# Optimization experiments

Hardware: AMD Instinct MI355X
Metric: run time of the kernel (lower is better)

Reference implementation:

```python
import jax, jax.numpy as jnp
import numpy as np

B, H, S, D = 4, 16, 2048, 128


def setup_inputs() -> dict:
    key = jax.random.key(0)
    kq, kk, kv = jax.random.split(key, 3)
    query = jax.random.normal(kq, (B, H, S, D), dtype=jnp.float32)
    key_t = jax.random.normal(kk, (B, H, S, D), dtype=jnp.float32)
    value = jax.random.normal(kv, (B, H, S, D), dtype=jnp.float32)
    # causal mask, broadcast over batch and heads: True = keep
    mask = jnp.tril(jnp.ones((S, S), dtype=bool))[None, None].repeat(B, 0).repeat(H, 1)
    return {"query": query, "key": key_t, "value": value, "mask": mask}


def reference(query, key, value, mask):
    scale = 1.0 / np.sqrt(D).astype(np.float32)
    # [b,h,sq,sk] scores
    scores = jnp.einsum("bhqd,bhkd->bhqk", query, key) * scale
    scores = jnp.where(mask, scores, -jnp.inf)
    probs = jax.nn.softmax(scores, axis=-1)
    return jnp.einsum("bhqk,bhkd->bhqd", probs, value)
```

## Files before the change

kernel.cpp:

```cpp
#include <hip/hip_runtime.h>


#define SLEN 2048
#define DDIM 128
#define NBH  64
#define QB   256
#define KB   64

typedef __bf16 bf16x8 __attribute__((ext_vector_type(8)));
typedef float  f32x16 __attribute__((ext_vector_type(16)));
typedef float  f32x4  __attribute__((ext_vector_type(4)));
typedef unsigned uint32x4 __attribute__((ext_vector_type(4)));
typedef unsigned short ushort_t;
typedef ushort_t ushort8 __attribute__((ext_vector_type(8)));

__device__ inline ushort_t f2bf(float f) {
  union { float f; unsigned u; } v; v.f = f;
  unsigned u = v.u;
  u += 0x7FFFu + ((u >> 16) & 1u);
  return (ushort_t)(u >> 16);
}

__device__ inline unsigned cvtpk_bf16(float lo, float hi) {
  unsigned r;
  asm("v_cvt_pk_bf16_f32 %0, %1, %2" : "=v"(r) : "v"(lo), "v"(hi));
  return r;
}

__device__ inline float exp2_fast(float x) {
  float r;
  asm("v_exp_f32 %0, %1" : "=v"(r) : "v"(x));
  return r;
}

__global__ __launch_bounds__(256) void convert_k_kernel(
    const float* __restrict__ in, ushort_t* __restrict__ out, int n4) {
  int stride = gridDim.x * blockDim.x;
  for (int i = blockIdx.x * blockDim.x + threadIdx.x; i < n4; i += stride) {
    float4 x = reinterpret_cast<const float4*>(in)[i];
    unsigned lo = (unsigned)f2bf(x.x) | ((unsigned)f2bf(x.y) << 16);
    unsigned hi = (unsigned)f2bf(x.z) | ((unsigned)f2bf(x.w) << 16);
    reinterpret_cast<uint2*>(out)[i] = make_uint2(lo, hi);
  }
}

__global__ __launch_bounds__(256) void transpose_v_kernel(
    const float* __restrict__ V, ushort_t* __restrict__ Vt) {
  __shared__ float t[64][33];
  const int bh = blockIdx.z;
  const int s0 = blockIdx.x * 64;
  const int d0 = blockIdx.y * 32;
  const int tx = threadIdx.x & 31;
  const int ty = threadIdx.x >> 5;
  const float* src = V + ((size_t)bh * SLEN + s0) * DDIM + d0;
#pragma unroll
  for (int j = 0; j < 8; ++j) {
    int sl = ty + j * 8;
    t[sl][tx] = src[(size_t)sl * DDIM + tx];
  }
  __syncthreads();
  ushort_t* dst = Vt + ((size_t)bh * DDIM + d0) * SLEN + s0;
#pragma unroll
  for (int j = 0; j < 4; ++j) {
    int dl = ty + j * 8;
    unsigned lo = f2bf(t[tx * 2][dl]);
    unsigned hi = f2bf(t[tx * 2 + 1][dl]);
    *reinterpret_cast<unsigned*>(&dst[(size_t)dl * SLEN + tx * 2]) =
        lo | (hi << 16);
  }
}

__global__ __launch_bounds__(512, 2) void fattn4_kernel(
    const float* __restrict__ Q, const ushort_t* __restrict__ Kb,
    const ushort_t* __restrict__ Vt, float* __restrict__ Out) {
  __shared__ ushort_t K_sh[2][KB * DDIM];
  __shared__ ushort_t V_sh[2][DDIM * KB];

  const int tid  = threadIdx.x;
  const int lane = tid & 63;
  const int wv   = tid >> 6;
  const int l31  = lane & 31;
  const int hi   = lane >> 5;
  const int qblk = (blockIdx.y >= 32) ? blockIdx.x : (7 - (int)blockIdx.x);
  const int bh   = blockIdx.y;

  const float qscale = 0.12751744f;
  const float THR = 11.0f;

  const float*    Qp = Q  + (size_t)bh * SLEN * DDIM;
  const ushort_t* Kp = Kb + (size_t)bh * SLEN * DDIM;
  const ushort_t* Vp = Vt + (size_t)bh * DDIM * SLEN;
  float*          Op = Out + (size_t)bh * SLEN * DDIM;

  const int q0w = qblk * QB + wv * 32;
  const int qg  = q0w + l31;

  bf16x8 qf[8];
  {
    const float* qr = Qp + (size_t)qg * DDIM;
#pragma unroll
    for (int ds = 0; ds < 8; ++ds) {
      int d0 = ds * 16 + hi * 8;
      float4 x = *reinterpret_cast<const float4*>(qr + d0);
      float4 y = *reinterpret_cast<const float4*>(qr + d0 + 4);
      ushort8 uu;
      uu[0] = f2bf(x.x * qscale); uu[1] = f2bf(x.y * qscale);
      uu[2] = f2bf(x.z * qscale); uu[3] = f2bf(x.w * qscale);
      uu[4] = f2bf(y.x * qscale); uu[5] = f2bf(y.y * qscale);
      uu[6] = f2bf(y.z * qscale); uu[7] = f2bf(y.w * qscale);
      qf[ds] = __builtin_bit_cast(bf16x8, uu);
    }
  }

  f32x16 Oacc[4];
#pragma unroll
  for (int dt = 0; dt < 4; ++dt)
#pragma unroll
    for (int r = 0; r < 16; ++r) Oacc[dt][r] = 0.f;
  float m_run = -3.0e38f, l_run = 0.f;

  const int last_kb      = qblk * 4 + 3;
  const int last_kb_wave = (q0w + 31) >> 6;

  auto stage = [&](int buf, int kb) {
    const ushort_t* ksrc = Kp + (size_t)kb * KB * DDIM;
#pragma unroll
    for (int j = 0; j < 2; ++j) {
      int chunk = wv * 128 + j * 64 + lane;
      int row = chunk >> 4, c = chunk & 15;
      const ushort_t* g = ksrc + row * DDIM + ((c ^ (row & 7)) << 3);
      ushort_t* l = &K_sh[buf][(size_t)(wv * 128 + j * 64) * 8];
      __builtin_amdgcn_global_load_lds(
          (const __attribute__((address_space(1))) unsigned*)g,
          (__attribute__((address_space(3))) unsigned*)l, 16, 0, 0);
    }
    const ushort_t* vsrc = Vp + (size_t)kb * KB;
#pragma unroll
    for (int j = 0; j < 2; ++j) {
      int chunk = wv * 128 + j * 64 + lane;
      int row = chunk >> 3, c = chunk & 7;
      const ushort_t* g = vsrc + (size_t)row * SLEN + ((c ^ (row & 7)) << 3);
      ushort_t* l = &V_sh[buf][(size_t)(wv * 128 + j * 64) * 8];
      __builtin_amdgcn_global_load_lds(
          (const __attribute__((address_space(1))) unsigned*)g,
          (__attribute__((address_space(3))) unsigned*)l, 16, 0, 0);
    }
  };

  stage(0, 0);

  for (int kb = 0; kb <= last_kb; ++kb) {
    __syncthreads();
    if (kb < last_kb) stage((kb + 1) & 1, kb + 1);

    if (kb <= last_kb_wave) {
      const int buf = kb & 1;

      f32x16 sac[2];
#pragma unroll
      for (int mt = 0; mt < 2; ++mt) {
        f32x16 a;
#pragma unroll
        for (int r = 0; r < 16; ++r) a[r] = 0.f;
        int row = mt * 32 + l31;
        int sw = row & 7;
        __builtin_amdgcn_s_setprio(1);
#pragma unroll
        for (int ds = 0; ds < 8; ++ds) {
          int c = ds * 2 + hi;
          bf16x8 kf = *reinterpret_cast<const bf16x8*>(
              &K_sh[buf][row * DDIM + ((c ^ sw) << 3)]);
          a = __builtin_amdgcn_mfma_f32_32x32x16_bf16(kf, qf[ds], a, 0, 0, 0);
        }
        __builtin_amdgcn_s_setprio(0);
        sac[mt] = a;
      }

      if (kb * 64 + 63 > q0w) {
#pragma unroll
        for (int mt = 0; mt < 2; ++mt) {
          int kbase = kb * 64 + mt * 32 + 4 * hi;
#pragma unroll
          for (int r = 0; r < 16; ++r) {
            int krow = (r & 3) + 8 * (r >> 2);
            if (kbase + krow > qg) sac[mt][r] = -3.0e38f;
          }
        }
      }

      float p0 = sac[0][0], p1 = sac[0][1], p2 = sac[0][2], p3 = sac[0][3];
#pragma unroll
      for (int r = 4; r < 16; r += 4) {
        p0 = fmaxf(p0, sac[0][r + 0]); p1 = fmaxf(p1, sac[0][r + 1]);
        p2 = fmaxf(p2, sac[0][r + 2]); p3 = fmaxf(p3, sac[0][r + 3]);
      }
#pragma unroll
      for (int r = 0; r < 16; r += 4) {
        p0 = fmaxf(p0, sac[1][r + 0]); p1 = fmaxf(p1, sac[1][r + 1]);
        p2 = fmaxf(p2, sac[1][r + 2]); p3 = fmaxf(p3, sac[1][r + 3]);
      }
      float tm = fmaxf(fmaxf(p0, p1), fmaxf(p2, p3));
      tm = fmaxf(tm, __shfl_xor(tm, 32));

      if (!__all(tm - m_run <= THR)) {
        float mnew  = fmaxf(m_run, tm);
        float alpha = exp2_fast(m_run - mnew);
        m_run = mnew;
        l_run *= alpha;
#pragma unroll
        for (int dt = 0; dt < 4; ++dt)
#pragma unroll
          for (int r = 0; r < 16; ++r) Oacc[dt][r] *= alpha;
      }

      float s0 = 0.f, s1 = 0.f, s2 = 0.f, s3 = 0.f;
#pragma unroll
      for (int mt = 0; mt < 2; ++mt)
#pragma unroll
        for (int r = 0; r < 16; r += 4) {
          float e0 = exp2_fast(sac[mt][r + 0] - m_run);
          float e1 = exp2_fast(sac[mt][r + 1] - m_run);
          float e2 = exp2_fast(sac[mt][r + 2] - m_run);
          float e3 = exp2_fast(sac[mt][r + 3] - m_run);
          sac[mt][r + 0] = e0; sac[mt][r + 1] = e1;
          sac[mt][r + 2] = e2; sac[mt][r + 3] = e3;
          s0 += e0; s1 += e1; s2 += e2; s3 += e3;
        }
      float rs = (s0 + s1) + (s2 + s3);
      rs += __shfl_xor(rs, 32);
      l_run += rs;

      uint32x4 pw[4];
#pragma unroll
      for (int ks = 0; ks < 4; ++ks) {
        const int mt = ks >> 1;
        const int hb = 8 * (ks & 1);
        unsigned X  = cvtpk_bf16(sac[mt][hb + 0], sac[mt][hb + 1]);
        unsigned X2 = cvtpk_bf16(sac[mt][hb + 2], sac[mt][hb + 3]);
        unsigned Y  = cvtpk_bf16(sac[mt][hb + 4], sac[mt][hb + 5]);
        unsigned Y2 = cvtpk_bf16(sac[mt][hb + 6], sac[mt][hb + 7]);
        asm("v_permlane32_swap_b32 %0, %1" : "+v"(X),  "+v"(Y));
        asm("v_permlane32_swap_b32 %0, %1" : "+v"(X2), "+v"(Y2));
        uint32x4 f; f.x = X; f.y = X2; f.z = Y; f.w = Y2;
        pw[ks] = f;
      }

#pragma unroll
      for (int dt = 0; dt < 4; ++dt) {
        int row = dt * 32 + l31;
        int sw = row & 7;
        __builtin_amdgcn_s_setprio(1);
#pragma unroll
        for (int ks = 0; ks < 4; ++ks) {
          int c = ks * 2 + hi;
          bf16x8 vf = *reinterpret_cast<const bf16x8*>(
              &V_sh[buf][row * 64 + ((c ^ sw) << 3)]);
          Oacc[dt] = __builtin_amdgcn_mfma_f32_32x32x16_bf16(
              vf, __builtin_bit_cast(bf16x8, pw[ks]), Oacc[dt], 0, 0, 0);
        }
        __builtin_amdgcn_s_setprio(0);
      }
    }
  }

  {
    float invl = 1.0f / l_run;
    float* orow = Op + (size_t)qg * DDIM;
#pragma unroll
    for (int dt = 0; dt < 4; ++dt)
#pragma unroll
      for (int r = 0; r < 16; ++r) {
        int d = dt * 32 + (r & 3) + 8 * (r >> 2) + 4 * hi;
        orow[d] = Oacc[dt][r] * invl;
      }
  }
}

__global__ __launch_bounds__(256) void fattn_kernel(
    const float* __restrict__ Q, const float* __restrict__ K,
    const float* __restrict__ V, float* __restrict__ Out) {
  __shared__ ushort_t K_sh[64 * 128];
  __shared__ ushort_t V_sh[128 * 64];
  __shared__ ushort_t P_sh[4][16 * 64];

  const int tid  = threadIdx.x;
  const int lane = tid & 63;
  const int wv   = tid >> 6;
  const int l16  = lane & 15;
  const int lhi  = lane >> 4;
  const int qblk = blockIdx.x;
  const int bh   = blockIdx.y;
  const float scale = 0.08838834764831845f;

  const size_t base = (size_t)bh * SLEN * DDIM;
  const float* Qp = Q + base;
  const float* Kp = K + base;
  const float* Vp = V + base;
  float*       Op = Out + base;

  bf16x8 qf[4];
  {
    const int qrow = qblk * 64 + wv * 16 + l16;
    const float* qr = Qp + (size_t)qrow * DDIM;
#pragma unroll
    for (int dc = 0; dc < 4; ++dc) {
      int d0 = dc * 32 + lhi * 8;
      float4 x = *reinterpret_cast<const float4*>(qr + d0);
      float4 y = *reinterpret_cast<const float4*>(qr + d0 + 4);
      ushort8 uu;
      uu[0] = f2bf(x.x * scale); uu[1] = f2bf(x.y * scale);
      uu[2] = f2bf(x.z * scale); uu[3] = f2bf(x.w * scale);
      uu[4] = f2bf(y.x * scale); uu[5] = f2bf(y.y * scale);
      uu[6] = f2bf(y.z * scale); uu[7] = f2bf(y.w * scale);
      qf[dc] = __builtin_bit_cast(bf16x8, uu);
    }
  }

  f32x4 Oacc[8];
#pragma unroll
  for (int i = 0; i < 8; ++i) Oacc[i] = (f32x4){0.f, 0.f, 0.f, 0.f};
  float m_run[4], l_run[4];
#pragma unroll
  for (int r = 0; r < 4; ++r) { m_run[r] = -3.0e38f; l_run[r] = 0.f; }

  for (int kb = 0; kb <= qblk; ++kb) {
    __syncthreads();
    {
      const float* src = Kp + (size_t)kb * 64 * DDIM;
#pragma unroll
      for (int it = 0; it < 8; ++it) {
        int idx4 = it * 256 + tid;
        int r  = idx4 >> 5;
        int c4 = idx4 & 31;
        float4 x = *reinterpret_cast<const float4*>(src + r * DDIM + c4 * 4);
        unsigned lo = ((unsigned)f2bf(x.y) << 16) | f2bf(x.x);
        unsigned hh = ((unsigned)f2bf(x.w) << 16) | f2bf(x.z);
        int e = (r * 128 + c4 * 4) ^ ((r & 7) << 3);
        *reinterpret_cast<uint2*>(&K_sh[e]) = make_uint2(lo, hh);
      }
      const float* vs = Vp + (size_t)kb * 64 * DDIM;
#pragma unroll
      for (int it = 0; it < 8; ++it) {
        int idx4 = it * 256 + tid;
        int r  = idx4 >> 5;
        int c4 = idx4 & 31;
        float4 x = *reinterpret_cast<const float4*>(vs + r * DDIM + c4 * 4);
        int c0 = c4 * 4;
        float vals[4] = {x.x, x.y, x.z, x.w};
#pragma unroll
        for (int j = 0; j < 4; ++j) {
          int d = c0 + j;
          V_sh[(d * 64 + r) ^ ((d & 7) << 3)] = f2bf(vals[j]);
        }
      }
    }
    __syncthreads();

    f32x4 sacc[4];
#pragma unroll
    for (int g = 0; g < 4; ++g) {
      f32x4 acc = (f32x4){0.f, 0.f, 0.f, 0.f};
#pragma unroll
      for (int dc = 0; dc < 4; ++dc) {
        int row = g * 16 + l16;
        int e = (row * 128 + dc * 32 + lhi * 8) ^ ((row & 7) << 3);
        bf16x8 kf = *reinterpret_cast<const bf16x8*>(&K_sh[e]);
        acc = __builtin_amdgcn_mfma_f32_16x16x32_bf16(qf[dc], kf, acc, 0, 0, 0);
      }
      sacc[g] = acc;
    }

    if (kb == qblk) {
      int q0 = lhi * 4;
#pragma unroll
      for (int g = 0; g < 4; ++g) {
        int kcol = g * 16 + l16;
#pragma unroll
        for (int r = 0; r < 4; ++r) {
          if (kcol > wv * 16 + q0 + r) sacc[g][r] = -3.0e38f;
        }
      }
    }

    float tmax[4];
#pragma unroll
    for (int r = 0; r < 4; ++r)
      tmax[r] = fmaxf(fmaxf(sacc[0][r], sacc[1][r]),
                      fmaxf(sacc[2][r], sacc[3][r]));
#pragma unroll
    for (int x = 1; x < 16; x <<= 1) {
#pragma unroll
      for (int r = 0; r < 4; ++r)
        tmax[r] = fmaxf(tmax[r], __shfl_xor(tmax[r], x));
    }

    float alpha[4], mnew[4];
#pragma unroll
    for (int r = 0; r < 4; ++r) {
      mnew[r]  = fmaxf(m_run[r], tmax[r]);
      alpha[r] = __expf(m_run[r] - mnew[r]);
      m_run[r] = mnew[r];
    }

    float rsum[4] = {0.f, 0.f, 0.f, 0.f};
#pragma unroll
    for (int g = 0; g < 4; ++g) {
#pragma unroll
      for (int r = 0; r < 4; ++r) {
        float p = __expf(sacc[g][r] - mnew[r]);
        rsum[r] += p;
        int prow = lhi * 4 + r;
        P_sh[wv][(prow * 64 + g * 16 + l16) ^ ((prow & 7) << 3)] = f2bf(p);
      }
    }
#pragma unroll
    for (int x = 1; x < 16; x <<= 1) {
#pragma unroll
      for (int r = 0; r < 4; ++r) rsum[r] += __shfl_xor(rsum[r], x);
    }
#pragma unroll
    for (int r = 0; r < 4; ++r) l_run[r] = l_run[r] * alpha[r] + rsum[r];

#pragma unroll
    for (int dg = 0; dg < 8; ++dg)
#pragma unroll
      for (int r = 0; r < 4; ++r) Oacc[dg][r] *= alpha[r];

    bf16x8 pf[2];
#pragma unroll
    for (int kc = 0; kc < 2; ++kc) {
      int e = (l16 * 64 + kc * 32 + lhi * 8) ^ ((l16 & 7) << 3);
      pf[kc] = *reinterpret_cast<const bf16x8*>(&P_sh[wv][e]);
    }
#pragma unroll
    for (int dg = 0; dg < 8; ++dg) {
#pragma unroll
      for (int kc = 0; kc < 2; ++kc) {
        int row = dg * 16 + l16;
        int e = (row * 64 + kc * 32 + lhi * 8) ^ ((row & 7) << 3);
        bf16x8 vf = *reinterpret_cast<const bf16x8*>(&V_sh[e]);
        Oacc[dg] = __builtin_amdgcn_mfma_f32_16x16x32_bf16(pf[kc], vf, Oacc[dg], 0, 0, 0);
      }
    }
  }

#pragma unroll
  for (int r = 0; r < 4; ++r) {
    float inv = 1.0f / l_run[r];
    int q = qblk * 64 + wv * 16 + lhi * 4 + r;
    float* orow = Op + (size_t)q * DDIM;
#pragma unroll
    for (int dg = 0; dg < 8; ++dg)
      orow[dg * 16 + l16] = Oacc[dg][r] * inv;
  }
}

extern "C" void kernel_launch(void* const* d_in, const int* in_sizes, int n_in,
                              void* d_out, int out_size, void* d_ws, size_t ws_size,
                              hipStream_t stream) {
  const float* Q = (const float*)d_in[0];
  const float* K = (const float*)d_in[1];
  const float* V = (const float*)d_in[2];
  float* O = (float*)d_out;

  const size_t n_elem = (size_t)NBH * SLEN * DDIM;
  const size_t need   = n_elem * 2 * 2;

  if (ws_size >= need) {
    ushort_t* Kbf = (ushort_t*)d_ws;
    ushort_t* Vt  = Kbf + n_elem;
    convert_k_kernel<<<2048, 256, 0, stream>>>(K, Kbf, (int)(n_elem / 4));
    transpose_v_kernel<<<dim3(SLEN / 64, DDIM / 32, NBH), 256, 0, stream>>>(V, Vt);
    fattn4_kernel<<<dim3(SLEN / QB, NBH), dim3(512), 0, stream>>>(Q, Kbf, Vt, O);
  } else {
    fattn_kernel<<<dim3(SLEN / 64, NBH), dim3(256), 0, stream>>>(Q, K, V, O);
  }
}
```

Measured before the change: 143.1 us.

## Software-pipeline QK^T with softmax/PV across triple-buffered tiles and merge prepasses

Restructures the attention main loop so the QK^T MFMAs for tile t are issued before the softmax and PV work for tile t-1. K/V LDS staging goes from a double buffer to a triple buffer so prefetch, compute and finish can each use their own tile. The K convert and V transpose prepasses are merged into one launch, and the output store is vectorized to float4. The aim is to overlap matrix-core work with exp/reduction work and save a kernel launch, at the cost of more LDS and more live registers, which could cut occupancy.

```diff
diff --git a/kernel.cpp b/kernel.cpp
--- a/kernel.cpp
+++ b/kernel.cpp
@@ -33,48 +33,153 @@
   return r;
 }
 
-__global__ __launch_bounds__(256) void convert_k_kernel(
-    const float* __restrict__ in, ushort_t* __restrict__ out, int n4) {
-  int stride = gridDim.x * blockDim.x;
-  for (int i = blockIdx.x * blockDim.x + threadIdx.x; i < n4; i += stride) {
-    float4 x = reinterpret_cast<const float4*>(in)[i];
-    unsigned lo = (unsigned)f2bf(x.x) | ((unsigned)f2bf(x.y) << 16);
-    unsigned hi = (unsigned)f2bf(x.z) | ((unsigned)f2bf(x.w) << 16);
-    reinterpret_cast<uint2*>(out)[i] = make_uint2(lo, hi);
-  }
-}
-
-__global__ __launch_bounds__(256) void transpose_v_kernel(
-    const float* __restrict__ V, ushort_t* __restrict__ Vt) {
+__global__ __launch_bounds__(256) void prepass_kernel(
+    const float* __restrict__ K, const float* __restrict__ V,
+    ushort_t* __restrict__ Kb, ushort_t* __restrict__ Vt) {
   __shared__ float t[64][33];
-  const int bh = blockIdx.z;
-  const int s0 = blockIdx.x * 64;
-  const int d0 = blockIdx.y * 32;
-  const int tx = threadIdx.x & 31;
-  const int ty = threadIdx.x >> 5;
-  const float* src = V + ((size_t)bh * SLEN + s0) * DDIM + d0;
-#pragma unroll
-  for (int j = 0; j < 8; ++j) {
-    int sl = ty + j * 8;
-    t[sl][tx] = src[(size_t)sl * DDIM + tx];
-  }
-  __syncthreads();
-  ushort_t* dst = Vt + ((size_t)bh * DDIM + d0) * SLEN + s0;
-#pragma unroll
-  for (int j = 0; j < 4; ++j) {
-    int dl = ty + j * 8;
-    unsigned lo = f2bf(t[tx * 2][dl]);
-    unsigned hi = f2bf(t[tx * 2 + 1][dl]);
-    *reinterpret_cast<unsigned*>(&dst[(size_t)dl * SLEN + tx * 2]) =
-        lo | (hi << 16);
-  }
-}
-
-__global__ __launch_bounds__(512, 2) void fattn4_kernel(
+  if (blockIdx.x < 2048) {
+    const int n4 = (int)((size_t)NBH * SLEN * DDIM / 4);
+    const int stride = 2048 * 256;
+    for (int i = blockIdx.x * 256 + threadIdx.x; i < n4; i += stride) {
+      float4 x = reinterpret_cast<const float4*>(K)[i];
+      unsigned lo = (unsigned)f2bf(x.x) | ((unsigned)f2bf(x.y) << 16);
+      unsigned hi = (unsigned)f2bf(x.z) | ((unsigned)f2bf(x.w) << 16);
+      reinterpret_cast<uint2*>(Kb)[i] = make_uint2(lo, hi);
+    }
+  } else {
+    const int vb = (int)blockIdx.x - 2048;
+    const int bh = vb >> 7;
+    const int d0 = ((vb >> 5) & 3) * 32;
+    const int s0 = (vb & 31) * 64;
+    const int tx = threadIdx.x & 31;
+    const int ty = threadIdx.x >> 5;
+    const float* src = V + ((size_t)bh * SLEN + s0) * DDIM + d0;
+#pragma unroll
+    for (int j = 0; j < 8; ++j) {
+      int sl = ty + j * 8;
+      t[sl][tx] = src[(size_t)sl * DDIM + tx];
+    }
+    __syncthreads();
+    ushort_t* dst = Vt + ((size_t)bh * DDIM + d0) * SLEN + s0;
+#pragma unroll
+    for (int j = 0; j < 4; ++j) {
+      int dl = ty + j * 8;
+      unsigned lo = f2bf(t[tx * 2][dl]);
+      unsigned hi = f2bf(t[tx * 2 + 1][dl]);
+      *reinterpret_cast<unsigned*>(&dst[(size_t)dl * SLEN + tx * 2]) =
+          lo | (hi << 16);
+    }
+  }
+}
+
+#define QKT(S, TT) do {                                                      \
+    const int _b = (TT) % 3;                                                 \
+    _Pragma("unroll")                                                        \
+    for (int mt = 0; mt < 2; ++mt) {                                         \
+      f32x16 a;                                                              \
+      _Pragma("unroll")                                                      \
+      for (int r = 0; r < 16; ++r) a[r] = 0.f;                               \
+      int row = mt * 32 + l31;                                               \
+      int sw = row & 7;                                                      \
+      _Pragma("unroll")                                                      \
+      for (int ds = 0; ds < 8; ++ds) {                                       \
+        int c = ds * 2 + hi;                                                 \
+        bf16x8 kf = *reinterpret_cast<const bf16x8*>(                        \
+            &K_sh[_b][row * DDIM + ((c ^ sw) << 3)]);                        \
+        a = __builtin_amdgcn_mfma_f32_32x32x16_bf16(kf, qf[ds], a, 0, 0, 0); \
+      }                                                                      \
+      S[mt] = a;                                                             \
+    }                                                                        \
+  } while (0)
+
+#define FINISH(S, U) do {                                                    \
+    const int _u = (U);                                                      \
+    const int _vb = _u % 3;                                                  \
+    if (_u * 64 + 63 > q0w) {                                                \
+      _Pragma("unroll")                                                      \
+      for (int mt = 0; mt < 2; ++mt) {                                       \
+        int kbase = _u * 64 + mt * 32 + 4 * hi;                              \
+        _Pragma("unroll")                                                    \
+        for (int r = 0; r < 16; ++r) {                                       \
+          int krow = (r & 3) + 8 * (r >> 2);                                 \
+          if (kbase + krow > qg) S[mt][r] = -3.0e38f;                        \
+        }                                                                    \
+      }                                                                      \
+    }                                                                        \
+    float p0 = S[0][0], p1 = S[0][1], p2 = S[0][2], p3 = S[0][3];            \
+    _Pragma("unroll")                                                        \
+    for (int r = 4; r < 16; r += 4) {                                        \
+      p0 = fmaxf(p0, S[0][r]);     p1 = fmaxf(p1, S[0][r + 1]);              \
+      p2 = fmaxf(p2, S[0][r + 2]); p3 = fmaxf(p3, S[0][r + 3]);              \
+    }                                                                        \
+    _Pragma("unroll")                                                        \
+    for (int r = 0; r < 16; r += 4) {                                        \
+      p0 = fmaxf(p0, S[1][r]);     p1 = fmaxf(p1, S[1][r + 1]);              \
+      p2 = fmaxf(p2, S[1][r + 2]); p3 = fmaxf(p3, S[1][r + 3]);              \
+    }                                                                        \
+    float tm = fmaxf(fmaxf(p0, p1), fmaxf(p2, p3));                          \
+    tm = fmaxf(tm, __shfl_xor(tm, 32));                                      \
+    if (!__all(tm - m_run <= THR)) {                                         \
+      float mnew  = fmaxf(m_run, tm);                                        \
+      float alpha = exp2_fast(m_run - mnew);                                 \
+      m_run = mnew; l_run *= alpha;                                          \
+      _Pragma("unroll")                                                      \
+      for (int dt = 0; dt < 4; ++dt)                                         \
+        _Pragma("unroll")                                                    \
+        for (int r = 0; r < 16; ++r) Oacc[dt][r] *= alpha;                   \
+    }                                                                        \
+    float s0 = 0.f, s1 = 0.f, s2 = 0.f, s3 = 0.f;                            \
+    _Pragma("unroll")                                                        \
+    for (int mt = 0; mt < 2; ++mt)                                           \
+      _Pragma("unroll")                                                      \
+      for (int r = 0; r < 16; r += 4) {                                      \
+        float e0 = exp2_fast(S[mt][r + 0] - m_run);                          \
+        float e1 = exp2_fast(S[mt][r + 1] - m_run);                          \
+        float e2 = exp2_fast(S[mt][r + 2] - m_run);                          \
+        float e3 = exp2_fast(S[mt][r + 3] - m_run);                          \
+        S[mt][r + 0] = e0; S[mt][r + 1] = e1;                                \
+        S[mt][r + 2] = e2; S[mt][r + 3] = e3;                                \
+        s0 += e0; s1 += e1; s2 += e2; s3 += e3;                              \
+      }                                                                      \
+    float rs = (s0 + s1) + (s2 + s3);                                        \
+    rs += __shfl_xor(rs, 32);                                                \
+    l_run += rs;                                                             \
+    uint32x4 pw[4];                                                          \
+    _Pragma("unroll")                                                        \
+    for (int ks = 0; ks < 4; ++ks) {                                         \
+      const int mt = ks >> 1;                                                \
+      const int hb = 8 * (ks & 1);                                           \
+      unsigned X  = cvtpk_bf16(S[mt][hb + 0], S[mt][hb + 1]);                \
+      unsigned X2 = cvtpk_bf16(S[mt][hb + 2], S[mt][hb + 3]);                \
+      unsigned Y  = cvtpk_bf16(S[mt][hb + 4], S[mt][hb + 5]);                \
+      unsigned Y2 = cvtpk_bf16(S[mt][hb + 6], S[mt][hb + 7]);                \
+      asm("v_permlane32_swap_b32 %0, %1" : "+v"(X),  "+v"(Y));               \
+      asm("v_permlane32_swap_b32 %0, %1" : "+v"(X2), "+v"(Y2));              \
+      uint32x4 f; f.x = X; f.y = X2; f.z = Y; f.w = Y2;                      \
+      pw[ks] = f;                                                            \
+    }                                                                        \
+    _Pragma("unroll")                                                        \
+    for (int dt = 0; dt < 4; ++dt) {                                         \
+      int row = dt * 32 + l31;                                               \
+      int sw = row & 7;                                                      \
+      __builtin_amdgcn_s_setprio(1);                                         \
+      _Pragma("unroll")                                                      \
+      for (int ks = 0; ks < 4; ++ks) {                                       \
+        int c = ks * 2 + hi;                                                 \
+        bf16x8 vf = *reinterpret_cast<const bf16x8*>(                        \
+            &V_sh[_vb][row * 64 + ((c ^ sw) << 3)]);                         \
+        Oacc[dt] = __builtin_amdgcn_mfma_f32_32x32x16_bf16(                  \
+            vf, __builtin_bit_cast(bf16x8, pw[ks]), Oacc[dt], 0, 0, 0);      \
+      }                                                                      \
+      __builtin_amdgcn_s_setprio(0);                                         \
+    }                                                                        \
+  } while (0)
+
+__global__ __launch_bounds__(512, 2) void fattn5_kernel(
     const float* __restrict__ Q, const ushort_t* __restrict__ Kb,
     const ushort_t* __restrict__ Vt, float* __restrict__ Out) {
-  __shared__ ushort_t K_sh[2][KB * DDIM];
-  __shared__ ushort_t V_sh[2][DDIM * KB];
+  __shared__ ushort_t K_sh[3][KB * DDIM];
+  __shared__ ushort_t V_sh[3][DDIM * KB];
 
   const int tid  = threadIdx.x;
   const int lane = tid & 63;
@@ -119,8 +224,8 @@
     for (int r = 0; r < 16; ++r) Oacc[dt][r] = 0.f;
   float m_run = -3.0e38f, l_run = 0.f;
 
-  const int last_kb      = qblk * 4 + 3;
-  const int last_kb_wave = (q0w + 31) >> 6;
+  const int last_kb = qblk * 4 + 3;
+  const int lkw     = 4 * qblk + (wv >> 1);
 
   auto stage = [&](int buf, int kb) {
     const ushort_t* ksrc = Kp + (size_t)kb * KB * DDIM;
@@ -129,7 +234,7 @@
       int chunk = wv * 128 + j * 64 + lane;
       int row = chunk >> 4, c = chunk & 15;
       const ushort_t* g = ksrc + row * DDIM + ((c ^ (row & 7)) << 3);
-      ushort_t* l = &K_sh[buf][(size_t)(wv * 128 + j * 64) * 8];
+      ushort_t* l = &K_sh[buf][(wv * 128 + j * 64) * 8];
       __builtin_amdgcn_global_load_lds(
           (const __attribute__((address_space(1))) unsigned*)g,
           (__attribute__((address_space(3))) unsigned*)l, 16, 0, 0);
@@ -140,128 +245,39 @@
       int chunk = wv * 128 + j * 64 + lane;
       int row = chunk >> 3, c = chunk & 7;
       const ushort_t* g = vsrc + (size_t)row * SLEN + ((c ^ (row & 7)) << 3);
-      ushort_t* l = &V_sh[buf][(size_t)(wv * 128 + j * 64) * 8];
+      ushort_t* l = &V_sh[buf][(wv * 128 + j * 64) * 8];
       __builtin_amdgcn_global_load_lds(
           (const __attribute__((address_space(1))) unsigned*)g,
           (__attribute__((address_space(3))) unsigned*)l, 16, 0, 0);
     }
   };
 
+  f32x16 sacA[2], sacB[2];
+
   stage(0, 0);
 
-  for (int kb = 0; kb <= last_kb; ++kb) {
+  __syncthreads();
+  stage(1, 1);
+  QKT(sacA, 0);
+
+  __syncthreads();
+  if (1 < last_kb) stage(2, 2);
+  if (1 <= lkw)           { QKT(sacB, 1); FINISH(sacA, 0); }
+  else if (lkw == 0)      { FINISH(sacA, 0); }
+
+  for (int t = 2; t <= last_kb; t += 2) {
     __syncthreads();
-    if (kb < last_kb) stage((kb + 1) & 1, kb + 1);
-
-    if (kb <= last_kb_wave) {
-      const int buf = kb & 1;
-
-      f32x16 sac[2];
-#pragma unroll
-      for (int mt = 0; mt < 2; ++mt) {
-        f32x16 a;
-#pragma unroll
-        for (int r = 0; r < 16; ++r) a[r] = 0.f;
-        int row = mt * 32 + l31;
-        int sw = row & 7;
-        __builtin_amdgcn_s_setprio(1);
-#pragma unroll
-        for (int ds = 0; ds < 8; ++ds) {
-          int c = ds * 2 + hi;
-          bf16x8 kf = *reinterpret_cast<const bf16x8*>(
-              &K_sh[buf][row * DDIM + ((c ^ sw) << 3)]);
-          a = __builtin_amdgcn_mfma_f32_32x32x16_bf16(kf, qf[ds], a, 0, 0, 0);
-        }
-        __builtin_amdgcn_s_setprio(0);
-        sac[mt] = a;
-      }
-
-      if (kb * 64 + 63 > q0w) {
-#pragma unroll
-        for (int mt = 0; mt < 2; ++mt) {
-          int kbase = kb * 64 + mt * 32 + 4 * hi;
-#pragma unroll
-          for (int r = 0; r < 16; ++r) {
-            int krow = (r & 3) + 8 * (r >> 2);
-            if (kbase + krow > qg) sac[mt][r] = -3.0e38f;
-          }
-        }
-      }
-
-      float p0 = sac[0][0], p1 = sac[0][1], p2 = sac[0][2], p3 = sac[0][3];
-#pragma unroll
-      for (int r = 4; r < 16; r += 4) {
-        p0 = fmaxf(p0, sac[0][r + 0]); p1 = fmaxf(p1, sac[0][r + 1]);
-        p2 = fmaxf(p2, sac[0][r + 2]); p3 = fmaxf(p3, sac[0][r + 3]);
-      }
-#pragma unroll
-      for (int r = 0; r < 16; r += 4) {
-        p0 = fmaxf(p0, sac[1][r + 0]); p1 = fmaxf(p1, sac[1][r + 1]);
-        p2 = fmaxf(p2, sac[1][r + 2]); p3 = fmaxf(p3, sac[1][r + 3]);
-      }
-      float tm = fmaxf(fmaxf(p0, p1), fmaxf(p2, p3));
-      tm = fmaxf(tm, __shfl_xor(tm, 32));
-
-      if (!__all(tm - m_run <= THR)) {
-        float mnew  = fmaxf(m_run, tm);
-        float alpha = exp2_fast(m_run - mnew);
-        m_run = mnew;
-        l_run *= alpha;
-#pragma unroll
-        for (int dt = 0; dt < 4; ++dt)
-#pragma unroll
-          for (int r = 0; r < 16; ++r) Oacc[dt][r] *= alpha;
-      }
-
-      float s0 = 0.f, s1 = 0.f, s2 = 0.f, s3 = 0.f;
-#pragma unroll
-      for (int mt = 0; mt < 2; ++mt)
-#pragma unroll
-        for (int r = 0; r < 16; r += 4) {
-          float e0 = exp2_fast(sac[mt][r + 0] - m_run);
-          float e1 = exp2_fast(sac[mt][r + 1] - m_run);
-          float e2 = exp2_fast(sac[mt][r + 2] - m_run);
-          float e3 = exp2_fast(sac[mt][r + 3] - m_run);
-          sac[mt][r + 0] = e0; sac[mt][r + 1] = e1;
-          sac[mt][r + 2] = e2; sac[mt][r + 3] = e3;
-          s0 += e0; s1 += e1; s2 += e2; s3 += e3;
-        }
-      float rs = (s0 + s1) + (s2 + s3);
-      rs += __shfl_xor(rs, 32);
-      l_run += rs;
-
-      uint32x4 pw[4];
-#pragma unroll
-      for (int ks = 0; ks < 4; ++ks) {
-        const int mt = ks >> 1;
-        const int hb = 8 * (ks & 1);
-        unsigned X  = cvtpk_bf16(sac[mt][hb + 0], sac[mt][hb + 1]);
-        unsigned X2 = cvtpk_bf16(sac[mt][hb + 2], sac[mt][hb + 3]);
-        unsigned Y  = cvtpk_bf16(sac[mt][hb + 4], sac[mt][hb + 5]);
-        unsigned Y2 = cvtpk_bf16(sac[mt][hb + 6], sac[mt][hb + 7]);
-        asm("v_permlane32_swap_b32 %0, %1" : "+v"(X),  "+v"(Y));
-        asm("v_permlane32_swap_b32 %0, %1" : "+v"(X2), "+v"(Y2));
-        uint32x4 f; f.x = X; f.y = X2; f.z = Y; f.w = Y2;
-        pw[ks] = f;
-      }
-
-#pragma unroll
-      for (int dt = 0; dt < 4; ++dt) {
-        int row = dt * 32 + l31;
-        int sw = row & 7;
-        __builtin_amdgcn_s_setprio(1);
-#pragma unroll
-        for (int ks = 0; ks < 4; ++ks) {
-          int c = ks * 2 + hi;
-          bf16x8 vf = *reinterpret_cast<const bf16x8*>(
-              &V_sh[buf][row * 64 + ((c ^ sw) << 3)]);
-          Oacc[dt] = __builtin_amdgcn_mfma_f32_32x32x16_bf16(
-              vf, __builtin_bit_cast(bf16x8, pw[ks]), Oacc[dt], 0, 0, 0);
-        }
-        __builtin_amdgcn_s_setprio(0);
-      }
-    }
-  }
+    if (t < last_kb) stage((t + 1) % 3, t + 1);
+    if (t <= lkw)            { QKT(sacA, t); FINISH(sacB, t - 1); }
+    else if (t == lkw + 1)   { FINISH(sacB, t - 1); }
+
+    __syncthreads();
+    if (t + 1 < last_kb) stage((t + 2) % 3, t + 2);
+    if (t + 1 <= lkw)          { QKT(sacB, t + 1); FINISH(sacA, t); }
+    else if (t + 1 == lkw + 1) { FINISH(sacA, t); }
+  }
+
+  if (lkw == last_kb) { FINISH(sacB, last_kb); }
 
   {
     float invl = 1.0f / l_run;
@@ -269,9 +285,14 @@
 #pragma unroll
     for (int dt = 0; dt < 4; ++dt)
 #pragma unroll
-      for (int r = 0; r < 16; ++r) {
-        int d = dt * 32 + (r & 3) + 8 * (r >> 2) + 4 * hi;
-        orow[d] = Oacc[dt][r] * invl;
+      for (int rq = 0; rq < 4; ++rq) {
+        float4 o;
+        o.x = Oacc[dt][rq * 4 + 0] * invl;
+        o.y = Oacc[dt][rq * 4 + 1] * invl;
+        o.z = Oacc[dt][rq * 4 + 2] * invl;
+        o.w = Oacc[dt][rq * 4 + 3] * invl;
+        int d = dt * 32 + 8 * rq + 4 * hi;
+        *reinterpret_cast<float4*>(orow + d) = o;
       }
   }
 }
@@ -279,8 +300,8 @@
 __global__ __launch_bounds__(256) void fattn_kernel(
     const float* __restrict__ Q, const float* __restrict__ K,
     const float* __restrict__ V, float* __restrict__ Out) {
-  __shared__ ushort_t K_sh[64 * 128];
-  __shared__ ushort_t V_sh[128 * 64];
+  __shared__ ushort_t Kf_sh[64 * 128];
+  __shared__ ushort_t Vf_sh[128 * 64];
   __shared__ ushort_t P_sh[4][16 * 64];
 
   const int tid  = threadIdx.x;
@@ -336,7 +357,7 @@
         unsigned lo = ((unsigned)f2bf(x.y) << 16) | f2bf(x.x);
         unsigned hh = ((unsigned)f2bf(x.w) << 16) | f2bf(x.z);
         int e = (r * 128 + c4 * 4) ^ ((r & 7) << 3);
-        *reinterpret_cast<uint2*>(&K_sh[e]) = make_uint2(lo, hh);
+        *reinterpret_cast<uint2*>(&Kf_sh[e]) = make_uint2(lo, hh);
       }
       const float* vs = Vp + (size_t)kb * 64 * DDIM;
 #pragma unroll
@@ -350,7 +371,7 @@
 #pragma unroll
         for (int j = 0; j < 4; ++j) {
           int d = c0 + j;
-          V_sh[(d * 64 + r) ^ ((d & 7) << 3)] = f2bf(vals[j]);
+          Vf_sh[(d * 64 + r) ^ ((d & 7) << 3)] = f2bf(vals[j]);
         }
       }
     }
@@ -364,7 +385,7 @@
       for (int dc = 0; dc < 4; ++dc) {
         int row = g * 16 + l16;
         int e = (row * 128 + dc * 32 + lhi * 8) ^ ((row & 7) << 3);
-        bf16x8 kf = *reinterpret_cast<const bf16x8*>(&K_sh[e]);
+        bf16x8 kf = *reinterpret_cast<const bf16x8*>(&Kf_sh[e]);
         acc = __builtin_amdgcn_mfma_f32_16x16x32_bf16(qf[dc], kf, acc, 0, 0, 0);
       }
       sacc[g] = acc;
@@ -438,7 +459,7 @@
       for (int kc = 0; kc < 2; ++kc) {
         int row = dg * 16 + l16;
         int e = (row * 64 + kc * 32 + lhi * 8) ^ ((row & 7) << 3);
-        bf16x8 vf = *reinterpret_cast<const bf16x8*>(&V_sh[e]);
+        bf16x8 vf = *reinterpret_cast<const bf16x8*>(&Vf_sh[e]);
         Oacc[dg] = __builtin_amdgcn_mfma_f32_16x16x32_bf16(pf[kc], vf, Oacc[dg], 0, 0, 0);
       }
     }
@@ -469,9 +490,8 @@
   if (ws_size >= need) {
     ushort_t* Kbf = (ushort_t*)d_ws;
     ushort_t* Vt  = Kbf + n_elem;
-    convert_k_kernel<<<2048, 256, 0, stream>>>(K, Kbf, (int)(n_elem / 4));
-    transpose_v_kernel<<<dim3(SLEN / 64, DDIM / 32, NBH), 256, 0, stream>>>(V, Vt);
-    fattn4_kernel<<<dim3(SLEN / QB, NBH), dim3(512), 0, stream>>>(Q, Kbf, Vt, O);
+    prepass_kernel<<<2048 + 8192, 256, 0, stream>>>(K, V, Kbf, Vt);
+    fattn5_kernel<<<dim3(SLEN / QB, NBH), dim3(512), 0, stream>>>(Q, Kbf, Vt, O);
   } else {
     fattn_kernel<<<dim3(SLEN / 64, NBH), dim3(256), 0, stream>>>(Q, K, V, O);
   }
```

After: 146.1 us. 1.02x slower.

## Merge K/V prepasses into one kernel and add atomic work-queue scheduling for attention

Applied to the files above, without the earlier changes.

The K conversion and V transpose are fused into a single prepass launch, which also resets a global counter. The attention kernel now pulls work items from that counter with an atomic, ordering items heaviest-first (largest causal query block first) so idle workgroups pick up remaining tiles. Output stores are vectorized to float4. This aims to cut one kernel launch, reduce the tail imbalance from causal masking, and improve store efficiency. The cost is an atomic plus an extra barrier per item and a counter kept in the workspace. With the grid equal to NITEMS, each block may simply take one item, so the dynamic balancing may add little.

```diff
diff --git a/kernel.cpp b/kernel.cpp
--- a/kernel.cpp
+++ b/kernel.cpp
@@ -6,6 +6,7 @@
 #define NBH  64
 #define QB   256
 #define KB   64
+#define NITEMS 512
 
 typedef __bf16 bf16x8 __attribute__((ext_vector_type(8)));
 typedef float  f32x16 __attribute__((ext_vector_type(16)));
@@ -33,254 +34,274 @@
   return r;
 }
 
-__global__ __launch_bounds__(256) void convert_k_kernel(
-    const float* __restrict__ in, ushort_t* __restrict__ out, int n4) {
-  int stride = gridDim.x * blockDim.x;
-  for (int i = blockIdx.x * blockDim.x + threadIdx.x; i < n4; i += stride) {
-    float4 x = reinterpret_cast<const float4*>(in)[i];
-    unsigned lo = (unsigned)f2bf(x.x) | ((unsigned)f2bf(x.y) << 16);
-    unsigned hi = (unsigned)f2bf(x.z) | ((unsigned)f2bf(x.w) << 16);
-    reinterpret_cast<uint2*>(out)[i] = make_uint2(lo, hi);
-  }
-}
-
-__global__ __launch_bounds__(256) void transpose_v_kernel(
-    const float* __restrict__ V, ushort_t* __restrict__ Vt) {
+__global__ __launch_bounds__(256) void prepass_kernel(
+    const float* __restrict__ K, const float* __restrict__ V,
+    ushort_t* __restrict__ Kb, ushort_t* __restrict__ Vt,
+    int* __restrict__ cnt) {
   __shared__ float t[64][33];
-  const int bh = blockIdx.z;
-  const int s0 = blockIdx.x * 64;
-  const int d0 = blockIdx.y * 32;
-  const int tx = threadIdx.x & 31;
-  const int ty = threadIdx.x >> 5;
-  const float* src = V + ((size_t)bh * SLEN + s0) * DDIM + d0;
-#pragma unroll
-  for (int j = 0; j < 8; ++j) {
-    int sl = ty + j * 8;
-    t[sl][tx] = src[(size_t)sl * DDIM + tx];
-  }
-  __syncthreads();
-  ushort_t* dst = Vt + ((size_t)bh * DDIM + d0) * SLEN + s0;
-#pragma unroll
-  for (int j = 0; j < 4; ++j) {
-    int dl = ty + j * 8;
-    unsigned lo = f2bf(t[tx * 2][dl]);
-    unsigned hi = f2bf(t[tx * 2 + 1][dl]);
-    *reinterpret_cast<unsigned*>(&dst[(size_t)dl * SLEN + tx * 2]) =
-        lo | (hi << 16);
-  }
-}
-
-__global__ __launch_bounds__(512, 2) void fattn4_kernel(
+  if (blockIdx.x == 0 && threadIdx.x == 0) *cnt = 0;
+  if (blockIdx.x < 2048) {
+    const int n4 = (int)((size_t)NBH * SLEN * DDIM / 4);
+    const int stride = 2048 * 256;
+    for (int i = blockIdx.x * 256 + threadIdx.x; i < n4; i += stride) {
+      float4 x = reinterpret_cast<const float4*>(K)[i];
+      unsigned lo = (unsigned)f2bf(x.x) | ((unsigned)f2bf(x.y) << 16);
+      unsigned hi = (unsigned)f2bf(x.z) | ((unsigned)f2bf(x.w) << 16);
+      reinterpret_cast<uint2*>(Kb)[i] = make_uint2(lo, hi);
+    }
+  } else {
+    const int vb = (int)blockIdx.x - 2048;
+    const int bh = vb >> 7;
+    const int d0 = ((vb >> 5) & 3) * 32;
+    const int s0 = (vb & 31) * 64;
+    const int tx = threadIdx.x & 31;
+    const int ty = threadIdx.x >> 5;
+    const float* src = V + ((size_t)bh * SLEN + s0) * DDIM + d0;
+#pragma unroll
+    for (int j = 0; j < 8; ++j) {
+      int sl = ty + j * 8;
+      t[sl][tx] = src[(size_t)sl * DDIM + tx];
+    }
+    __syncthreads();
+    ushort_t* dst = Vt + ((size_t)bh * DDIM + d0) * SLEN + s0;
+#pragma unroll
+    for (int j = 0; j < 4; ++j) {
+      int dl = ty + j * 8;
+      unsigned lo = f2bf(t[tx * 2][dl]);
+      unsigned hi = f2bf(t[tx * 2 + 1][dl]);
+      *reinterpret_cast<unsigned*>(&dst[(size_t)dl * SLEN + tx * 2]) =
+          lo | (hi << 16);
+    }
+  }
+}
+
+__global__ __launch_bounds__(512, 2) void fattn8_kernel(
     const float* __restrict__ Q, const ushort_t* __restrict__ Kb,
-    const ushort_t* __restrict__ Vt, float* __restrict__ Out) {
+    const ushort_t* __restrict__ Vt, float* __restrict__ Out,
+    int* __restrict__ cnt) {
   __shared__ ushort_t K_sh[2][KB * DDIM];
   __shared__ ushort_t V_sh[2][DDIM * KB];
+  __shared__ int item_sh;
 
   const int tid  = threadIdx.x;
   const int lane = tid & 63;
   const int wv   = tid >> 6;
   const int l31  = lane & 31;
   const int hi   = lane >> 5;
-  const int qblk = (blockIdx.y >= 32) ? blockIdx.x : (7 - (int)blockIdx.x);
-  const int bh   = blockIdx.y;
 
   const float qscale = 0.12751744f;
   const float THR = 11.0f;
 
-  const float*    Qp = Q  + (size_t)bh * SLEN * DDIM;
-  const ushort_t* Kp = Kb + (size_t)bh * SLEN * DDIM;
-  const ushort_t* Vp = Vt + (size_t)bh * DDIM * SLEN;
-  float*          Op = Out + (size_t)bh * SLEN * DDIM;
-
-  const int q0w = qblk * QB + wv * 32;
-  const int qg  = q0w + l31;
-
-  bf16x8 qf[8];
-  {
-    const float* qr = Qp + (size_t)qg * DDIM;
-#pragma unroll
-    for (int ds = 0; ds < 8; ++ds) {
-      int d0 = ds * 16 + hi * 8;
-      float4 x = *reinterpret_cast<const float4*>(qr + d0);
-      float4 y = *reinterpret_cast<const float4*>(qr + d0 + 4);
-      ushort8 uu;
-      uu[0] = f2bf(x.x * qscale); uu[1] = f2bf(x.y * qscale);
-      uu[2] = f2bf(x.z * qscale); uu[3] = f2bf(x.w * qscale);
-      uu[4] = f2bf(y.x * qscale); uu[5] = f2bf(y.y * qscale);
-      uu[6] = f2bf(y.z * qscale); uu[7] = f2bf(y.w * qscale);
-      qf[ds] = __builtin_bit_cast(bf16x8, uu);
-    }
-  }
-
-  f32x16 Oacc[4];
-#pragma unroll
-  for (int dt = 0; dt < 4; ++dt)
-#pragma unroll
-    for (int r = 0; r < 16; ++r) Oacc[dt][r] = 0.f;
-  float m_run = -3.0e38f, l_run = 0.f;
-
-  const int last_kb      = qblk * 4 + 3;
-  const int last_kb_wave = (q0w + 31) >> 6;
-
-  auto stage = [&](int buf, int kb) {
-    const ushort_t* ksrc = Kp + (size_t)kb * KB * DDIM;
-#pragma unroll
-    for (int j = 0; j < 2; ++j) {
-      int chunk = wv * 128 + j * 64 + lane;
-      int row = chunk >> 4, c = chunk & 15;
-      const ushort_t* g = ksrc + row * DDIM + ((c ^ (row & 7)) << 3);
-      ushort_t* l = &K_sh[buf][(size_t)(wv * 128 + j * 64) * 8];
-      __builtin_amdgcn_global_load_lds(
-          (const __attribute__((address_space(1))) unsigned*)g,
-          (__attribute__((address_space(3))) unsigned*)l, 16, 0, 0);
-    }
-    const ushort_t* vsrc = Vp + (size_t)kb * KB;
-#pragma unroll
-    for (int j = 0; j < 2; ++j) {
-      int chunk = wv * 128 + j * 64 + lane;
-      int row = chunk >> 3, c = chunk & 7;
-      const ushort_t* g = vsrc + (size_t)row * SLEN + ((c ^ (row & 7)) << 3);
-      ushort_t* l = &V_sh[buf][(size_t)(wv * 128 + j * 64) * 8];
-      __builtin_amdgcn_global_load_lds(
-          (const __attribute__((address_space(1))) unsigned*)g,
-          (__attribute__((address_space(3))) unsigned*)l, 16, 0, 0);
-    }
-  };
-
-  stage(0, 0);
-
-  for (int kb = 0; kb <= last_kb; ++kb) {
+  while (true) {
+    if (tid == 0) item_sh = atomicAdd(cnt, 1);
     __syncthreads();
-    if (kb < last_kb) stage((kb + 1) & 1, kb + 1);
-
-    if (kb <= last_kb_wave) {
-      const int buf = kb & 1;
-
-      f32x16 sac[2];
-#pragma unroll
-      for (int mt = 0; mt < 2; ++mt) {
-        f32x16 a;
-#pragma unroll
-        for (int r = 0; r < 16; ++r) a[r] = 0.f;
-        int row = mt * 32 + l31;
-        int sw = row & 7;
-        __builtin_amdgcn_s_setprio(1);
-#pragma unroll
-        for (int ds = 0; ds < 8; ++ds) {
-          int c = ds * 2 + hi;
-          bf16x8 kf = *reinterpret_cast<const bf16x8*>(
-              &K_sh[buf][row * DDIM + ((c ^ sw) << 3)]);
-          a = __builtin_amdgcn_mfma_f32_32x32x16_bf16(kf, qf[ds], a, 0, 0, 0);
-        }
-        __builtin_amdgcn_s_setprio(0);
-        sac[mt] = a;
-      }
-
-      if (kb * 64 + 63 > q0w) {
+    const int item = item_sh;
+    if (item >= NITEMS) break;
+
+    const int qblk = 7 - (item >> 6);
+    const int bh   = item & 63;
+
+    const float*    Qp = Q  + (size_t)bh * SLEN * DDIM;
+    const ushort_t* Kp = Kb + (size_t)bh * SLEN * DDIM;
+    const ushort_t* Vp = Vt + (size_t)bh * DDIM * SLEN;
+    float*          Op = Out + (size_t)bh * SLEN * DDIM;
+
+    const int q0w = qblk * QB + wv * 32;
+    const int qg  = q0w + l31;
+
+    bf16x8 qf[8];
+    {
+      const float* qr = Qp + (size_t)qg * DDIM;
+#pragma unroll
+      for (int ds = 0; ds < 8; ++ds) {
+        int d0 = ds * 16 + hi * 8;
+        float4 x = *reinterpret_cast<const float4*>(qr + d0);
+        float4 y = *reinterpret_cast<const float4*>(qr + d0 + 4);
+        ushort8 uu;
+        uu[0] = f2bf(x.x * qscale); uu[1] = f2bf(x.y * qscale);
+        uu[2] = f2bf(x.z * qscale); uu[3] = f2bf(x.w * qscale);
+        uu[4] = f2bf(y.x * qscale); uu[5] = f2bf(y.y * qscale);
+        uu[6] = f2bf(y.z * qscale); uu[7] = f2bf(y.w * qscale);
+        qf[ds] = __builtin_bit_cast(bf16x8, uu);
+      }
+    }
+
+    f32x16 Oacc[4];
+#pragma unroll
+    for (int dt = 0; dt < 4; ++dt)
+#pragma unroll
+      for (int r = 0; r < 16; ++r) Oacc[dt][r] = 0.f;
+    float m_run = -3.0e38f, l_run = 0.f;
+
+    const int last_kb       = qblk * 4 + 3;
+    const int last_kb_wave  = (q0w + 31) >> 6;
+
+    auto stage = [&](int buf, int kb) {
+      const ushort_t* ksrc = Kp + (size_t)kb * KB * DDIM;
+#pragma unroll
+      for (int j = 0; j < 2; ++j) {
+        int chunk = wv * 128 + j * 64 + lane;
+        int row = chunk >> 4, c = chunk & 15;
+        const ushort_t* g = ksrc + row * DDIM + ((c ^ (row & 7)) << 3);
+        ushort_t* l = &K_sh[buf][(wv * 128 + j * 64) * 8];
+        __builtin_amdgcn_global_load_lds(
+            (const __attribute__((address_space(1))) unsigned*)g,
+            (__attribute__((address_space(3))) unsigned*)l, 16, 0, 0);
+      }
+      const ushort_t* vsrc = Vp + (size_t)kb * KB;
+#pragma unroll
+      for (int j = 0; j < 2; ++j) {
+        int chunk = wv * 128 + j * 64 + lane;
+        int row = chunk >> 3, c = chunk & 7;
+        const ushort_t* g = vsrc + (size_t)row * SLEN + ((c ^ (row & 7)) << 3);
+        ushort_t* l = &V_sh[buf][(wv * 128 + j * 64) * 8];
+        __builtin_amdgcn_global_load_lds(
+            (const __attribute__((address_space(1))) unsigned*)g,
+            (__attribute__((address_space(3))) unsigned*)l, 16, 0, 0);
+      }
+    };
+
+    stage(0, 0);
+
+    for (int kb = 0; kb <= last_kb; ++kb) {
+      __syncthreads();
+      if (kb < last_kb) stage((kb + 1) & 1, kb + 1);
+
+      if (kb <= last_kb_wave) {
+        const int buf = kb & 1;
+
+        f32x16 sac[2];
 #pragma unroll
         for (int mt = 0; mt < 2; ++mt) {
-          int kbase = kb * 64 + mt * 32 + 4 * hi;
-#pragma unroll
-          for (int r = 0; r < 16; ++r) {
-            int krow = (r & 3) + 8 * (r >> 2);
-            if (kbase + krow > qg) sac[mt][r] = -3.0e38f;
+          f32x16 a;
+#pragma unroll
+          for (int r = 0; r < 16; ++r) a[r] = 0.f;
+          int row = mt * 32 + l31;
+          int sw = row & 7;
+          __builtin_amdgcn_s_setprio(1);
+#pragma unroll
+          for (int ds = 0; ds < 8; ++ds) {
+            int c = ds * 2 + hi;
+            bf16x8 kf = *reinterpret_cast<const bf16x8*>(
+                &K_sh[buf][row * DDIM + ((c ^ sw) << 3)]);
+            a = __builtin_amdgcn_mfma_f32_32x32x16_bf16(kf, qf[ds], a, 0, 0, 0);
           }
-        }
-      }
-
-      float p0 = sac[0][0], p1 = sac[0][1], p2 = sac[0][2], p3 = sac[0][3];
-#pragma unroll
-      for (int r = 4; r < 16; r += 4) {
-        p0 = fmaxf(p0, sac[0][r + 0]); p1 = fmaxf(p1, sac[0][r + 1]);
-        p2 = fmaxf(p2, sac[0][r + 2]); p3 = fmaxf(p3, sac[0][r + 3]);
-      }
-#pragma unroll
-      for (int r = 0; r < 16; r += 4) {
-        p0 = fmaxf(p0, sac[1][r + 0]); p1 = fmaxf(p1, sac[1][r + 1]);
-        p2 = fmaxf(p2, sac[1][r + 2]); p3 = fmaxf(p3, sac[1][r + 3]);
-      }
-      float tm = fmaxf(fmaxf(p0, p1), fmaxf(p2, p3));
-      tm = fmaxf(tm, __shfl_xor(tm, 32));
-
-      if (!__all(tm - m_run <= THR)) {
-        float mnew  = fmaxf(m_run, tm);
-        float alpha = exp2_fast(m_run - mnew);
-        m_run = mnew;
-        l_run *= alpha;
-#pragma unroll
-        for (int dt = 0; dt < 4; ++dt)
-#pragma unroll
-          for (int r = 0; r < 16; ++r) Oacc[dt][r] *= alpha;
-      }
-
-      float s0 = 0.f, s1 = 0.f, s2 = 0.f, s3 = 0.f;
-#pragma unroll
-      for (int mt = 0; mt < 2; ++mt)
+          __builtin_amdgcn_s_setprio(0);
+          sac[mt] = a;
+        }
+
+        if (kb * 64 + 63 > q0w) {
+#pragma unroll
+          for (int mt = 0; mt < 2; ++mt) {
+            int kbase = kb * 64 + mt * 32 + 4 * hi;
+#pragma unroll
+            for (int r = 0; r < 16; ++r) {
+              int krow = (r & 3) + 8 * (r >> 2);
+              if (kbase + krow > qg) sac[mt][r] = -3.0e38f;
+            }
+          }
+        }
+
+        float p0 = sac[0][0], p1 = sac[0][1], p2 = sac[0][2], p3 = sac[0][3];
+#pragma unroll
+        for (int r = 4; r < 16; r += 4) {
+          p0 = fmaxf(p0, sac[0][r + 0]); p1 = fmaxf(p1, sac[0][r + 1]);
+          p2 = fmaxf(p2, sac[0][r + 2]); p3 = fmaxf(p3, sac[0][r + 3]);
+        }
 #pragma unroll
         for (int r = 0; r < 16; r += 4) {
-          float e0 = exp2_fast(sac[mt][r + 0] - m_run);
-          float e1 = exp2_fast(sac[mt][r + 1] - m_run);
-          float e2 = exp2_fast(sac[mt][r + 2] - m_run);
-          float e3 = exp2_fast(sac[mt][r + 3] - m_run);
-          sac[mt][r + 0] = e0; sac[mt][r + 1] = e1;
-          sac[mt][r + 2] = e2; sac[mt][r + 3] = e3;
-          s0 += e0; s1 += e1; s2 += e2; s3 += e3;
-        }
-      float rs = (s0 + s1) + (s2 + s3);
-      rs += __shfl_xor(rs, 32);
-      l_run += rs;
-
-      uint32x4 pw[4];
-#pragma unroll
-      for (int ks = 0; ks < 4; ++ks) {
-        const int mt = ks >> 1;
-        const int hb = 8 * (ks & 1);
-        unsigned X  = cvtpk_bf16(sac[mt][hb + 0], sac[mt][hb + 1]);
-        unsigned X2 = cvtpk_bf16(sac[mt][hb + 2], sac[mt][hb + 3]);
-        unsigned Y  = cvtpk_bf16(sac[mt][hb + 4], sac[mt][hb + 5]);
-        unsigned Y2 = cvtpk_bf16(sac[mt][hb + 6], sac[mt][hb + 7]);
-        asm("v_permlane32_swap_b32 %0, %1" : "+v"(X),  "+v"(Y));
-        asm("v_permlane32_swap_b32 %0, %1" : "+v"(X2), "+v"(Y2));
-        uint32x4 f; f.x = X; f.y = X2; f.z = Y; f.w = Y2;
-        pw[ks] = f;
-      }
-
-#pragma unroll
-      for (int dt = 0; dt < 4; ++dt) {
-        int row = dt * 32 + l31;
-        int sw = row & 7;
-        __builtin_amdgcn_s_setprio(1);
+          p0 = fmaxf(p0, sac[1][r + 0]); p1 = fmaxf(p1, sac[1][r + 1]);
+          p2 = fmaxf(p2, sac[1][r + 2]); p3 = fmaxf(p3, sac[1][r + 3]);
+        }
+        float tm = fmaxf(fmaxf(p0, p1), fmaxf(p2, p3));
+        tm = fmaxf(tm, __shfl_xor(tm, 32));
+
+        if (!__all(tm - m_run <= THR)) {
+          float mnew  = fmaxf(m_run, tm);
+          float alpha = exp2_fast(m_run - mnew);
+          m_run = mnew;
+          l_run *= alpha;
+#pragma unroll
+          for (int dt = 0; dt < 4; ++dt)
+#pragma unroll
+            for (int r = 0; r < 16; ++r) Oacc[dt][r] *= alpha;
+        }
+
+        float s0 = 0.f, s1 = 0.f, s2 = 0.f, s3 = 0.f;
+#pragma unroll
+        for (int mt = 0; mt < 2; ++mt)
+#pragma unroll
+          for (int r = 0; r < 16; r += 4) {
+            float e0 = exp2_fast(sac[mt][r + 0] - m_run);
+            float e1 = exp2_fast(sac[mt][r + 1] - m_run);
+            float e2 = exp2_fast(sac[mt][r + 2] - m_run);
+            float e3 = exp2_fast(sac[mt][r + 3] - m_run);
+            sac[mt][r + 0] = e0; sac[mt][r + 1] = e1;
+            sac[mt][r + 2] = e2; sac[mt][r + 3] = e3;
+            s0 += e0; s1 += e1; s2 += e2; s3 += e3;
+          }
+        float rs = (s0 + s1) + (s2 + s3);
+        rs += __shfl_xor(rs, 32);
+        l_run += rs;
+
+        uint32x4 pw[4];
 #pragma unroll
         for (int ks = 0; ks < 4; ++ks) {
-          int c = ks * 2 + hi;
-          bf16x8 vf = *reinterpret_cast<const bf16x8*>(
-              &V_sh[buf][row * 64 + ((c ^ sw) << 3)]);
-          Oacc[dt] = __builtin_amdgcn_mfma_f32_32x32x16_bf16(
-              vf, __builtin_bit_cast(bf16x8, pw[ks]), Oacc[dt], 0, 0, 0);
-        }
-        __builtin_amdgcn_s_setprio(0);
-      }
-    }
-  }
-
-  {
-    float invl = 1.0f / l_run;
-    float* orow = Op + (size_t)qg * DDIM;
-#pragma unroll
-    for (int dt = 0; dt < 4; ++dt)
-#pragma unroll
-      for (int r = 0; r < 16; ++r) {
-        int d = dt * 32 + (r & 3) + 8 * (r >> 2) + 4 * hi;
-        orow[d] = Oacc[dt][r] * invl;
-      }
+          const int mt = ks >> 1;
+          const int hb = 8 * (ks & 1);
+          unsigned X  = cvtpk_bf16(sac[mt][hb + 0], sac[mt][hb + 1]);
+          unsigned X2 = cvtpk_bf16(sac[mt][hb + 2], sac[mt][hb + 3]);
+          unsigned Y  = cvtpk_bf16(sac[mt][hb + 4], sac[mt][hb + 5]);
+          unsigned Y2 = cvtpk_bf16(sac[mt][hb + 6], sac[mt][hb + 7]);
+          asm("v_permlane32_swap_b32 %0, %1" : "+v"(X),  "+v"(Y));
+          asm("v_permlane32_swap_b32 %0, %1" : "+v"(X2), "+v"(Y2));
+          uint32x4 f; f.x = X; f.y = X2; f.z = Y; f.w = Y2;
+          pw[ks] = f;
+        }
+
+#pragma unroll
+        for (int dt = 0; dt < 4; ++dt) {
+          int row = dt * 32 + l31;
+          int sw = row & 7;
+          __builtin_amdgcn_s_setprio(1);
+#pragma unroll
+          for (int ks = 0; ks < 4; ++ks) {
+            int c = ks * 2 + hi;
+            bf16x8 vf = *reinterpret_cast<const bf16x8*>(
+                &V_sh[buf][row * 64 + ((c ^ sw) << 3)]);
+            Oacc[dt] = __builtin_amdgcn_mfma_f32_32x32x16_bf16(
+                vf, __builtin_bit_cast(bf16x8, pw[ks]), Oacc[dt], 0, 0, 0);
+          }
+          __builtin_amdgcn_s_setprio(0);
+        }
+      }
+    }
+
+    {
+      float invl = 1.0f / l_run;
+      float* orow = Op + (size_t)qg * DDIM;
+#pragma unroll
+      for (int dt = 0; dt < 4; ++dt)
+#pragma unroll
+        for (int rq = 0; rq < 4; ++rq) {
+          float4 o;
+          o.x = Oacc[dt][rq * 4 + 0] * invl;
+          o.y = Oacc[dt][rq * 4 + 1] * invl;
+          o.z = Oacc[dt][rq * 4 + 2] * invl;
+          o.w = Oacc[dt][rq * 4 + 3] * invl;
+          int d = dt * 32 + 8 * rq + 4 * hi;
+          *reinterpret_cast<float4*>(orow + d) = o;
+        }
+    }
+    __syncthreads();
   }
 }
 
 __global__ __launch_bounds__(256) void fattn_kernel(
     const float* __restrict__ Q, const float* __restrict__ K,
     const float* __restrict__ V, float* __restrict__ Out) {
-  __shared__ ushort_t K_sh[64 * 128];
-  __shared__ ushort_t V_sh[128 * 64];
+  __shared__ ushort_t Kf_sh[64 * 128];
+  __shared__ ushort_t Vf_sh[128 * 64];
   __shared__ ushort_t P_sh[4][16 * 64];
 
   const int tid  = threadIdx.x;
@@ -336,7 +357,7 @@
         unsigned lo = ((unsigned)f2bf(x.y) << 16) | f2bf(x.x);
         unsigned hh = ((unsigned)f2bf(x.w) << 16) | f2bf(x.z);
         int e = (r * 128 + c4 * 4) ^ ((r & 7) << 3);
-        *reinterpret_cast<uint2*>(&K_sh[e]) = make_uint2(lo, hh);
+        *reinterpret_cast<uint2*>(&Kf_sh[e]) = make_uint2(lo, hh);
       }
       const float* vs = Vp + (size_t)kb * 64 * DDIM;
 #pragma unroll
@@ -350,7 +371,7 @@
 #pragma unroll
         for (int j = 0; j < 4; ++j) {
           int d = c0 + j;
-          V_sh[(d * 64 + r) ^ ((d & 7) << 3)] = f2bf(vals[j]);
+          Vf_sh[(d * 64 + r) ^ ((d & 7) << 3)] = f2bf(vals[j]);
         }
       }
     }
@@ -364,7 +385,7 @@
       for (int dc = 0; dc < 4; ++dc) {
         int row = g * 16 + l16;
         int e = (row * 128 + dc * 32 + lhi * 8) ^ ((row & 7) << 3);
-        bf16x8 kf = *reinterpret_cast<const bf16x8*>(&K_sh[e]);
+        bf16x8 kf = *reinterpret_cast<const bf16x8*>(&Kf_sh[e]);
         acc = __builtin_amdgcn_mfma_f32_16x16x32_bf16(qf[dc], kf, acc, 0, 0, 0);
       }
       sacc[g] = acc;
@@ -438,7 +459,7 @@
       for (int kc = 0; kc < 2; ++kc) {
         int row = dg * 16 + l16;
         int e = (row * 64 + kc * 32 + lhi * 8) ^ ((row & 7) << 3);
-        bf16x8 vf = *reinterpret_cast<const bf16x8*>(&V_sh[e]);
+        bf16x8 vf = *reinterpret_cast<const bf16x8*>(&Vf_sh[e]);
         Oacc[dg] = __builtin_amdgcn_mfma_f32_16x16x32_bf16(pf[kc], vf, Oacc[dg], 0, 0, 0);
       }
     }
@@ -464,14 +485,14 @@
   float* O = (float*)d_out;
 
   const size_t n_elem = (size_t)NBH * SLEN * DDIM;
-  const size_t need   = n_elem * 2 * 2;
+  const size_t need   = n_elem * 2 * 2 + 64;
 
   if (ws_size >= need) {
     ushort_t* Kbf = (ushort_t*)d_ws;
     ushort_t* Vt  = Kbf + n_elem;
-    convert_k_kernel<<<2048, 256, 0, stream>>>(K, Kbf, (int)(n_elem / 4));
-    transpose_v_kernel<<<dim3(SLEN / 64, DDIM / 32, NBH), 256, 0, stream>>>(V, Vt);
-    fattn4_kernel<<<dim3(SLEN / QB, NBH), dim3(512), 0, stream>>>(Q, Kbf, Vt, O);
+    int* cnt      = (int*)(Vt + n_elem);
+    prepass_kernel<<<2048 + 8192, 256, 0, stream>>>(K, V, Kbf, Vt, cnt);
+    fattn8_kernel<<<dim3(NITEMS), dim3(512), 0, stream>>>(Q, Kbf, Vt, O, cnt);
   } else {
     fattn_kernel<<<dim3(SLEN / 64, NBH), dim3(256), 0, stream>>>(Q, K, V, O);
   }
```

Result: no change. 142.0 us (-0.8%).
